# Optimization experiments

Measured on AMD Instinct MI355X. Metric: run time of the kernel, lower is better.

Reference implementation:

```python
import jax, jax.numpy as jnp
import numpy as np

# Config from the repo: 128^3 volume, patch 2 -> 64^3 patches, embed_dim 64
D = H = W = 64
C = 64
WS = 2        # window_size
SS = 1        # shift_size
NH = 8        # num_heads
MLP = 256     # num_mlp
B = 2
L = D * H * W
S = WS ** 3   # tokens per window = 8
NUM_REL = (2 * WS - 1) ** 3  # 27


def _rel_position_index(ws):
    # faithful to source, incl. np.meshgrid default 'xy' indexing
    coords = np.stack(np.meshgrid(np.arange(ws), np.arange(ws), np.arange(ws)))
    cf = coords.reshape(3, -1)
    rc = (cf[:, :, None] - cf[:, None, :]).transpose(1, 2, 0)
    rc[:, :, 0] += ws - 1
    rc[:, :, 1] += ws - 1
    rc[:, :, 2] += ws - 1
    rc[:, :, 0] *= 2 * ws - 1
    return rc.sum(-1)  # (S, S) int


def _attn_mask(d, h, w, ws, ss):
    sl = (slice(0, -ws), slice(-ws, -ss), slice(-ss, None))
    m = np.zeros((1, d, h, w, 1), np.float32)
    cnt = 0
    for ds in sl:
        for hs in sl:
            for wsl in sl:
                m[:, ds, hs, wsl, :] = cnt
                cnt += 1
    pz, py, px = d // ws, h // ws, w // ws
    mw = m.reshape(1, pz, ws, py, ws, px, ws, 1)
    mw = mw.transpose(0, 1, 3, 5, 2, 4, 6, 7).reshape(-1, ws ** 3)  # (nW, S)
    am = mw[:, None, :] - mw[:, :, None]
    return np.where(am != 0, -100.0, 0.0).astype(np.float32)  # (nW, S, S)


_REL_IDX = _rel_position_index(WS).reshape(-1)          # (S*S,)
_MASK = _attn_mask(D, H, W, WS, SS)                     # (nW, S, S)


def setup_inputs() -> dict:
    key = jax.random.key(0)
    ks = jax.random.split(key, 8)
    n = lambda k, s: jax.random.normal(k, s, jnp.float32) * 0.02
    return {
        "x": jax.random.normal(ks[0], (B, L, C), jnp.float32),
        "norm1_g": jnp.ones((C,), jnp.float32),
        "norm1_b": jnp.zeros((C,), jnp.float32),
        "qkv_w": n(ks[1], (C, 3 * C)),
        "qkv_b": jnp.zeros((3 * C,), jnp.float32),
        "rpb": n(ks[2], (NUM_REL, NH)),
        "proj_w": n(ks[3], (C, C)),
        "proj_b": jnp.zeros((C,), jnp.float32),
        "norm2_g": jnp.ones((C,), jnp.float32),
        "norm2_b": jnp.zeros((C,), jnp.float32),
        "mlp_w1": n(ks[4], (C, MLP)),
        "mlp_b1": jnp.zeros((MLP,), jnp.float32),
        "mlp_w2": n(ks[5], (MLP, C)),
        "mlp_b2": jnp.zeros((C,), jnp.float32),
    }


def _ln(x, g, b, eps=1e-5):
    mu = jnp.mean(x, -1, keepdims=True)
    var = jnp.mean(jnp.square(x - mu), -1, keepdims=True)
    return (x - mu) * jax.lax.rsqrt(var + eps) * g + b


def _forward(x, norm1_g, norm1_b, qkv_w, qkv_b, rpb, proj_w, proj_b,
             norm2_g, norm2_b, mlp_w1, mlp_b1, mlp_w2, mlp_b2):
    b = x.shape[0]
    pz, py, px = D // WS, H // WS, W // WS
    hd = C // NH
    scale = hd ** -0.5

    h = _ln(x, norm1_g, norm1_b).reshape(b, D, H, W, C)
    h = jnp.roll(h, (-SS, -SS, -SS), (1, 2, 3))  # cyclic shift
    # window partition -> (b*nW, S, C)
    w = h.reshape(b, pz, WS, py, WS, px, WS, C)
    w = w.transpose(0, 1, 3, 5, 2, 4, 6, 7).reshape(-1, S, C)
    n = w.shape[0]

    qkv = (w @ qkv_w + qkv_b).reshape(n, S, 3, NH, hd).transpose(2, 0, 3, 1, 4)
    q, k, v = qkv[0] * scale, qkv[1], qkv[2]   # (n, NH, S, hd)
    attn = jnp.einsum('nhqd,nhkd->nhqk', q, k)  # (n, NH, S, S)

    # relative position bias, gather + reshape exactly as in the source
    bias = rpb[jnp.asarray(_REL_IDX)].reshape(S, S, S, -1).transpose(3, 0, 1, 2)
    attn = attn + bias  # broadcasts since NH == S == 8 in this config

    mask = jnp.asarray(_MASK)  # (nW, S, S)
    nW = mask.shape[0]
    attn = attn.reshape(-1, nW, NH, S, S) + mask[None, :, None]
    attn = jax.nn.softmax(attn.reshape(-1, NH, S, S), axis=-1)

    out = jnp.einsum('nhqk,nhkd->nhqd', attn, v)
    out = out.transpose(0, 2, 1, 3).reshape(n, S, C)
    out = out @ proj_w + proj_b

    # window reverse (bug-faithful to the source's reshape/transpose order)
    xr = out.reshape(-1, pz, WS, py, px, WS, WS, C)
    xr = xr.transpose(0, 1, 3, 5, 2, 4, 6, 7).reshape(-1, D, H, W, C)
    xr = jnp.roll(xr, (SS, SS, SS), (1, 2, 3))
    h = xr.reshape(b, L, C)

    x = x + h  # DropPath/Dropout are identity in eval mode
    skip = x
    h = _ln(x, norm2_g, norm2_b)
    h = jax.nn.gelu(h @ mlp_w1 + mlp_b1, approximate=False) @ mlp_w2 + mlp_b2
    return skip + h


def reference(x, norm1_g, norm1_b, qkv_w, qkv_b, rpb, proj_w, proj_b,
              norm2_g, norm2_b, mlp_w1, mlp_b1, mlp_w2, mlp_b2):
    return _forward(x, norm1_g, norm1_b, qkv_w, qkv_b, rpb, proj_w, proj_b,
                    norm2_g, norm2_b, mlp_w1, mlp_b1, mlp_w2, mlp_b2)
```

## Files before the change

kernel.cpp:

```cpp
#include <hip/hip_runtime.h>
#include <math.h>

typedef unsigned short u16;
typedef unsigned int u32;
typedef __attribute__((ext_vector_type(8))) short short8;
typedef __attribute__((ext_vector_type(4))) float f32x4;

__device__ __forceinline__ float bf2f(u16 u) {
  union { u32 i; float f; } v; v.i = ((u32)u) << 16; return v.f;
}
__device__ __forceinline__ u16 f2bf(float f) {
  union { float f; u32 i; } v; v.f = f;
  u32 i = v.i;
  i += 0x7fffu + ((i >> 16) & 1u);
  return (u16)(i >> 16);
}

template<bool F32>
__device__ __forceinline__ float ld(const void* p, int i) {
  if (F32) return ((const float*)p)[i];
  return bf2f(((const u16*)p)[i]);
}

__global__ __launch_bounds__(64)
void detect_kernel(const void* __restrict__ xv, int* __restrict__ flag) {
  const u32* xw = (const u32*)xv;
  const int t = threadIdx.x;
  int bad = 0;
  for (int i = t; i < 1024; i += 64) {
    const int e = (int)((xw[i] >> 7) & 0xFF);
    if (e < 90 || e > 150) bad++;
  }
#pragma unroll
  for (int m = 1; m < 64; m <<= 1) bad += __shfl_xor(bad, m);
  if (t == 0) *flag = (bad > 256) ? 1 : 0;
}

template<bool F32>
__device__ __forceinline__ void gather8(const void* __restrict__ x, int chunk,
                                        int w, int s, int cg, float* pf) {
  const int b     = chunk >> 13;
  const int wbase = (chunk & 8191) << 2;
  const int widx  = wbase + w;
  const int wz = widx >> 10, wy = (widx >> 5) & 31, wx = widx & 31;
  const int od = (2*wz + ((s>>2)&1) + 1) & 63;
  const int oh = (2*wy + ((s>>1)&1) + 1) & 63;
  const int ow = (2*wx + ( s    &1) + 1) & 63;
  const int base = (((b<<18) + ((od<<12)|(oh<<6)|ow)) << 6) + cg*8;
  if (F32) {
    const f32x4 a = *(const f32x4*)((const float*)x + base);
    const f32x4 c = *(const f32x4*)((const float*)x + base + 4);
    pf[0]=a[0]; pf[1]=a[1]; pf[2]=a[2]; pf[3]=a[3];
    pf[4]=c[0]; pf[5]=c[1]; pf[6]=c[2]; pf[7]=c[3];
  } else {
    const short8 a = *(const short8*)((const u16*)x + base);
#pragma unroll
    for (int j = 0; j < 8; ++j) pf[j] = bf2f((u16)a[j]);
  }
}

__device__ __forceinline__ int scat(int chunk, int tok) {
  const int b     = chunk >> 13;
  const int wbase = (chunk & 8191) << 2;
  const int widx = wbase + (tok >> 3);
  const int s    = tok & 7;
  const int wz = widx >> 10, wy = (widx >> 5) & 31, wx = widx & 31;
  const int fd = (2*wz + ((wy>>3)&1) + 1) & 63;
  const int Hb = 8*(wy&7) + 4*(wx>>4) + (wy>>4);
  const int Wb = 4*(wx&15);
  const int i = (s>>2)&1, j = (s>>1)&1, k = s&1;
  const int fh = (Hb + 2*j + 1) & 63;
  const int fw = (Wb + 2*i + k + 1) & 63;
  return ((b<<18) + ((fd<<12)|(fh<<6)|fw)) << 6;
}

#define MFMA __builtin_amdgcn_mfma_f32_16x16x32_bf16

template<bool F32>
__device__ __forceinline__ void attn_body(
    const void* __restrict__ x,
    const void* __restrict__ n1g, const void* __restrict__ n1b,
    const void* __restrict__ qkvw, const void* __restrict__ qkvb,
    const void* __restrict__ rpb,
    const void* __restrict__ projw, const void* __restrict__ projb,
    float* __restrict__ out,
    u16* __restrict__ aL, u16* __restrict__ qL,
    u16* __restrict__ kL, u16* __restrict__ vL)
{
  const int tid  = threadIdx.x;
  const int w    = tid >> 6, l = tid & 63;
  const int quad = l >> 4,  col = l & 15;
  const int s8   = l >> 3,  cg  = l & 7;

  float g1v[8], be1v[8];
#pragma unroll
  for (int j = 0; j < 8; ++j) {
    g1v[j]  = ld<F32>(n1g, cg*8 + j);
    be1v[j] = ld<F32>(n1b, cg*8 + j);
  }

  short8 bq[3][2];
#pragma unroll
  for (int nt = 0; nt < 3; ++nt)
#pragma unroll
    for (int kt = 0; kt < 2; ++kt) {
      short8 f;
#pragma unroll
      for (int j = 0; j < 8; ++j)
        f[j] = (short)f2bf(ld<F32>(qkvw, (kt*32 + quad*8 + j)*192 + w*48 + nt*16 + col));
      bq[nt][kt] = f;
    }
  float qb[3];
#pragma unroll
  for (int nt = 0; nt < 3; ++nt) qb[nt] = ld<F32>(qkvb, w*48 + nt*16 + col);
  short8 bp[2];
#pragma unroll
  for (int kt = 0; kt < 2; ++kt) {
    short8 f;
#pragma unroll
    for (int j = 0; j < 8; ++j)
      f[j] = (short)f2bf(ld<F32>(projw, (kt*32 + quad*8 + j)*64 + w*16 + col));
    bp[kt] = f;
  }
  const float pbv = ld<F32>(projb, w*16 + col);
  const int rel = 3 * (((s8>>1)&1) - ((cg>>1)&1) + 1)
                +     (((s8>>2)&1) - ((cg>>2)&1) + 1)
                +     (( s8    &1) - ( cg    &1) + 1);
  float rpv[8];
#pragma unroll
  for (int kk = 0; kk < 8; ++kk) rpv[kk] = ld<F32>(rpb, rel*8 + kk);

  float pf[8];
  gather8<F32>(x, blockIdx.x, w, s8, cg, pf);

  for (int chunk = blockIdx.x; chunk < 16384; chunk += 2048) {
    const int wbase = (chunk & 8191) << 2;
    const int widx0 = wbase + w;
    const int wz0 = widx0 >> 10, wy0 = (widx0 >> 5) & 31, wx0 = widx0 & 31;

    {
      float s1 = 0.f, sq = 0.f;
#pragma unroll
      for (int j = 0; j < 8; ++j) { s1 += pf[j]; sq += pf[j]*pf[j]; }
#pragma unroll
      for (int m = 1; m < 8; m <<= 1) {
        s1 += __shfl_xor(s1, m);
        sq += __shfl_xor(sq, m);
      }
      const float mu  = s1 * 0.015625f;
      const float var = sq * 0.015625f - mu * mu;
      const float rs  = rsqrtf(var + 1e-5f);
      short8 av;
#pragma unroll
      for (int j = 0; j < 8; ++j)
        av[j] = (short)f2bf((pf[j] - mu) * rs * g1v[j] + be1v[j]);
      *(short8*)&aL[(w*8 + s8)*72 + cg*8] = av;
    }
    if (chunk + 2048 < 16384) gather8<F32>(x, chunk + 2048, w, s8, cg, pf);
    __syncthreads();

    {
      short8 aF[2][2];
#pragma unroll
      for (int mt = 0; mt < 2; ++mt)
#pragma unroll
        for (int kt = 0; kt < 2; ++kt)
          aF[mt][kt] = *(const short8*)&aL[(mt*16 + col)*72 + kt*32 + quad*8];
#pragma unroll
      for (int nt = 0; nt < 3; ++nt) {
        f32x4 a0 = (f32x4){0.f,0.f,0.f,0.f}, a1 = (f32x4){0.f,0.f,0.f,0.f};
        a0 = MFMA(aF[0][0], bq[nt][0], a0, 0, 0, 0);
        a0 = MFMA(aF[0][1], bq[nt][1], a0, 0, 0, 0);
        a1 = MFMA(aF[1][0], bq[nt][0], a1, 0, 0, 0);
        a1 = MFMA(aF[1][1], bq[nt][1], a1, 0, 0, 0);
        const int nb  = w*48 + nt*16;
        u16* dst      = (nb < 64) ? qL : (nb < 128) ? kL : vL;
        const int chb = (nb & 63) + col;
        const float scl = (nb < 64) ? 0.35355339059327373f : 1.0f;
        const float bb  = qb[nt];
#pragma unroll
        for (int r = 0; r < 4; ++r) {
          dst[(quad*4 + r)*72 + chb]      = f2bf((a0[r] + bb) * scl);
          dst[(16 + quad*4 + r)*72 + chb] = f2bf((a1[r] + bb) * scl);
        }
      }
    }
    __syncthreads();

    {
      const int tq = w*8 + cg;
      float qr[8];
      {
        const short8 qv = *(const short8*)&qL[tq*72 + s8*8];
#pragma unroll
        for (int d = 0; d < 8; ++d) qr[d] = bf2f((u16)qv[d]);
      }
      float sc8[8];
#pragma unroll
      for (int kk = 0; kk < 8; ++kk) {
        const short8 kv = *(const short8*)&kL[(w*8 + kk)*72 + s8*8];
        float a = 0.f;
#pragma unroll
        for (int d = 0; d < 8; ++d) a += qr[d] * bf2f((u16)kv[d]);
        sc8[kk] = a + rpv[kk];
      }
      {
        int cnts[8];
#pragma unroll
        for (int p = 0; p < 8; ++p) {
          const int sd = 2*wz0 + ((p>>2)&1);
          const int sh = 2*wy0 + ((p>>1)&1);
          const int sw = 2*wx0 + (p&1);
          cnts[p] = (sd >= 62 ? sd - 61 : 0)*9 + (sh >= 62 ? sh - 61 : 0)*3
                  + (sw >= 62 ? sw - 61 : 0);
        }
#pragma unroll
        for (int kk = 0; kk < 8; ++kk)
          if (cnts[kk] != cnts[cg]) sc8[kk] -= 100.f;
      }
      float mx = sc8[0];
#pragma unroll
      for (int kk = 1; kk < 8; ++kk) mx = fmaxf(mx, sc8[kk]);
      float pr[8], lsum = 0.f;
#pragma unroll
      for (int kk = 0; kk < 8; ++kk) { pr[kk] = __expf(sc8[kk] - mx); lsum += pr[kk]; }
      const float inv = __builtin_amdgcn_rcpf(lsum);
      float o[8];
#pragma unroll
      for (int d = 0; d < 8; ++d) o[d] = 0.f;
#pragma unroll
      for (int kk = 0; kk < 8; ++kk) {
        const short8 vv = *(const short8*)&vL[(w*8 + kk)*72 + s8*8];
#pragma unroll
        for (int d = 0; d < 8; ++d) o[d] += pr[kk] * bf2f((u16)vv[d]);
      }
      short8 ov;
#pragma unroll
      for (int d = 0; d < 8; ++d) ov[d] = (short)f2bf(o[d] * inv);
      *(short8*)&qL[tq*72 + s8*8] = ov;
    }
    int offs[8]; float xr[8];
#pragma unroll
    for (int mt = 0; mt < 2; ++mt)
#pragma unroll
      for (int r = 0; r < 4; ++r) {
        const int off = scat(chunk, mt*16 + quad*4 + r) + w*16 + col;
        offs[mt*4 + r] = off;
        xr[mt*4 + r]   = ld<F32>(x, off);
      }
    __syncthreads();

    {
      f32x4 c0 = (f32x4){0.f,0.f,0.f,0.f}, c1 = (f32x4){0.f,0.f,0.f,0.f};
      c0 = MFMA(*(const short8*)&qL[(col)*72 + quad*8],         bp[0], c0, 0, 0, 0);
      c0 = MFMA(*(const short8*)&qL[(col)*72 + 32 + quad*8],    bp[1], c0, 0, 0, 0);
      c1 = MFMA(*(const short8*)&qL[(16+col)*72 + quad*8],      bp[0], c1, 0, 0, 0);
      c1 = MFMA(*(const short8*)&qL[(16+col)*72 + 32 + quad*8], bp[1], c1, 0, 0, 0);
#pragma unroll
      for (int r = 0; r < 4; ++r) {
        out[offs[r]]     = xr[r]     + c0[r] + pbv;
        out[offs[4 + r]] = xr[4 + r] + c1[r] + pbv;
      }
    }
    __syncthreads();
  }
}

__global__ __launch_bounds__(256, 4)
void attn_kernel(const void* __restrict__ x,
                 const void* __restrict__ n1g, const void* __restrict__ n1b,
                 const void* __restrict__ qkvw, const void* __restrict__ qkvb,
                 const void* __restrict__ rpb,
                 const void* __restrict__ projw, const void* __restrict__ projb,
                 const int* __restrict__ flag, float* __restrict__ out)
{
  __shared__ __align__(16) u16 aL[32*72];
  __shared__ __align__(16) u16 qL[32*72];
  __shared__ __align__(16) u16 kL[32*72];
  __shared__ __align__(16) u16 vL[32*72];
  if (*flag)
    attn_body<true >(x, n1g, n1b, qkvw, qkvb, rpb, projw, projb, out, aL, qL, kL, vL);
  else
    attn_body<false>(x, n1g, n1b, qkvw, qkvb, rpb, projw, projb, out, aL, qL, kL, vL);
}

template<bool F32>
__device__ __forceinline__ void mlp_body(
    float* __restrict__ io,
    const void* __restrict__ n2g, const void* __restrict__ n2b,
    const void* __restrict__ mw1, const void* __restrict__ mb1,
    const void* __restrict__ mw2, const void* __restrict__ mb2,
    u16* __restrict__ aL, u16* __restrict__ hL, float* __restrict__ yL)
{
  const int tid  = threadIdx.x;
  const int w    = tid >> 6, l = tid & 63;
  const int quad = l >> 4,  col = l & 15;
  const int s8   = l >> 3,  cg  = l & 7;
  const int ltok = w*8 + s8;
  const int chunk = blockIdx.x;

  float pf[8];
  {
    const float* p = &io[(chunk*32 + ltok)*64 + cg*8];
    const f32x4 a = *(const f32x4*)p;
    const f32x4 c = *(const f32x4*)(p + 4);
    pf[0]=a[0]; pf[1]=a[1]; pf[2]=a[2]; pf[3]=a[3];
    pf[4]=c[0]; pf[5]=c[1]; pf[6]=c[2]; pf[7]=c[3];
  }

  float g2v[8], be2v[8];
#pragma unroll
  for (int j = 0; j < 8; ++j) {
    g2v[j]  = ld<F32>(n2g, cg*8 + j);
    be2v[j] = ld<F32>(n2b, cg*8 + j);
  }
  float b1vv[4];
#pragma unroll
  for (int nt = 0; nt < 4; ++nt) b1vv[nt] = ld<F32>(mb1, w*64 + nt*16 + col);
  const float b2vv = ld<F32>(mb2, w*16 + col);

  short8 b1f[2][4];
#pragma unroll
  for (int kt = 0; kt < 2; ++kt)
#pragma unroll
    for (int nt = 0; nt < 4; ++nt) {
      short8 f;
#pragma unroll
      for (int j = 0; j < 8; ++j)
        f[j] = (short)f2bf(ld<F32>(mw1, (kt*32 + quad*8 + j)*256 + w*64 + nt*16 + col));
      b1f[kt][nt] = f;
    }

  {
    float s1 = 0.f, sq = 0.f;
#pragma unroll
    for (int j = 0; j < 8; ++j) { s1 += pf[j]; sq += pf[j]*pf[j]; }
#pragma unroll
    for (int m = 1; m < 8; m <<= 1) {
      s1 += __shfl_xor(s1, m);
      sq += __shfl_xor(sq, m);
    }
    const float mu  = s1 * 0.015625f;
    const float var = sq * 0.015625f - mu * mu;
    const float rs  = rsqrtf(var + 1e-5f);
    short8 av;
#pragma unroll
    for (int j = 0; j < 8; ++j)
      av[j] = (short)f2bf((pf[j] - mu) * rs * g2v[j] + be2v[j]);
    *(short8*)&aL[ltok*72 + cg*8] = av;
    *(f32x4*)&yL[ltok*68 + cg*8]     = (f32x4){pf[0], pf[1], pf[2], pf[3]};
    *(f32x4*)&yL[ltok*68 + cg*8 + 4] = (f32x4){pf[4], pf[5], pf[6], pf[7]};
  }
  __syncthreads();

  {
    short8 aF[2][2];
#pragma unroll
    for (int mt = 0; mt < 2; ++mt)
#pragma unroll
      for (int kt = 0; kt < 2; ++kt)
        aF[mt][kt] = *(const short8*)&aL[(mt*16 + col)*72 + kt*32 + quad*8];
#pragma unroll
    for (int nt = 0; nt < 4; ++nt) {
      f32x4 m0 = (f32x4){0.f,0.f,0.f,0.f}, m1 = (f32x4){0.f,0.f,0.f,0.f};
      m0 = MFMA(aF[0][0], b1f[0][nt], m0, 0, 0, 0);
      m0 = MFMA(aF[0][1], b1f[1][nt], m0, 0, 0, 0);
      m1 = MFMA(aF[1][0], b1f[0][nt], m1, 0, 0, 0);
      m1 = MFMA(aF[1][1], b1f[1][nt], m1, 0, 0, 0);
      const float bb = b1vv[nt];
#pragma unroll
      for (int r = 0; r < 4; ++r) {
        {
          const float h = m0[r] + bb;
          const float u = h * (1.5957691216f + 0.0713548162f * (h * h));
          const float e = __expf(u);
          hL[(quad*4 + r)*264 + w*64 + nt*16 + col] =
              f2bf(h - h * __builtin_amdgcn_rcpf(e + 1.f));
        }
        {
          const float h = m1[r] + bb;
          const float u = h * (1.5957691216f + 0.0713548162f * (h * h));
          const float e = __expf(u);
          hL[(16 + quad*4 + r)*264 + w*64 + nt*16 + col] =
              f2bf(h - h * __builtin_amdgcn_rcpf(e + 1.f));
        }
      }
    }
  }

  short8 b2f[8];
#pragma unroll
  for (int kt = 0; kt < 8; ++kt) {
    short8 f;
#pragma unroll
    for (int j = 0; j < 8; ++j)
      f[j] = (short)f2bf(ld<F32>(mw2, (kt*32 + quad*8 + j)*64 + w*16 + col));
    b2f[kt] = f;
  }
  __syncthreads();

  {
    f32x4 o0 = (f32x4){0.f,0.f,0.f,0.f}, o1 = (f32x4){0.f,0.f,0.f,0.f};
#pragma unroll
    for (int kt = 0; kt < 8; ++kt) {
      o0 = MFMA(*(const short8*)&hL[(col)*264 + kt*32 + quad*8],    b2f[kt], o0, 0, 0, 0);
      o1 = MFMA(*(const short8*)&hL[(16+col)*264 + kt*32 + quad*8], b2f[kt], o1, 0, 0, 0);
    }
#pragma unroll
    for (int r = 0; r < 4; ++r) {
      const int r0 = quad*4 + r, r1 = 16 + quad*4 + r;
      io[(chunk*32 + r0)*64 + w*16 + col] = yL[r0*68 + w*16 + col] + o0[r] + b2vv;
      io[(chunk*32 + r1)*64 + w*16 + col] = yL[r1*68 + w*16 + col] + o1[r] + b2vv;
    }
  }
}

__global__ __launch_bounds__(256, 4)
void mlp_kernel(float* __restrict__ io,
                const void* __restrict__ n2g, const void* __restrict__ n2b,
                const void* __restrict__ mw1, const void* __restrict__ mb1,
                const void* __restrict__ mw2, const void* __restrict__ mb2,
                const int* __restrict__ flag)
{
  __shared__ __align__(16) u16   aL[32 * 72];
  __shared__ __align__(16) u16   hL[32 * 264];
  __shared__ __align__(16) float yL[32 * 68];
  if (*flag)
    mlp_body<true >(io, n2g, n2b, mw1, mb1, mw2, mb2, aL, hL, yL);
  else
    mlp_body<false>(io, n2g, n2b, mw1, mb1, mw2, mb2, aL, hL, yL);
}

extern "C" void kernel_launch(void* const* d_in, const int* in_sizes, int n_in,
                              void* d_out, int out_size, void* d_ws, size_t ws_size,
                              hipStream_t stream) {
  const void* x     = d_in[0];
  const void* n1g   = d_in[1];
  const void* n1b   = d_in[2];
  const void* qkvw  = d_in[3];
  const void* qkvb  = d_in[4];
  const void* rpb   = d_in[5];
  const void* projw = d_in[6];
  const void* projb = d_in[7];
  const void* n2g   = d_in[8];
  const void* n2b   = d_in[9];
  const void* mw1   = d_in[10];
  const void* mb1   = d_in[11];
  const void* mw2   = d_in[12];
  const void* mb2   = d_in[13];
  float* out = (float*)d_out;
  int* flag  = (int*)d_ws;

  detect_kernel<<<dim3(1), dim3(64), 0, stream>>>(x, flag);
  attn_kernel<<<dim3(2048), dim3(256), 0, stream>>>(
      x, n1g, n1b, qkvw, qkvb, rpb, projw, projb, flag, out);
  mlp_kernel<<<dim3(16384), dim3(256), 0, stream>>>(
      out, n2g, n2b, mw1, mb1, mw2, mb2, flag);
}
```

Before: 459.1 us.

## Prepack MLP weights to bf16 fragments and move residual add into MLP

```diff
diff --git a/kernel.cpp b/kernel.cpp
--- a/kernel.cpp
+++ b/kernel.cpp
@@ -34,6 +34,34 @@
 #pragma unroll
   for (int m = 1; m < 64; m <<= 1) bad += __shfl_xor(bad, m);
   if (t == 0) *flag = (bad > 256) ? 1 : 0;
+}
+
+template<bool F32>
+__device__ __forceinline__ void pack_body(const void* __restrict__ mw1,
+                                          const void* __restrict__ mw2,
+                                          u16* __restrict__ wsb1,
+                                          u16* __restrict__ wsb2) {
+  const int g  = blockIdx.x * 256 + threadIdx.x;
+  const int gs = gridDim.x * 256;
+  for (int e = g; e < 16384; e += gs) {
+    const int j = e & 7, l = (e >> 3) & 63, nt = (e >> 9) & 3,
+              kt = (e >> 11) & 1, w = e >> 12;
+    const int quad = l >> 4, col = l & 15;
+    wsb1[e] = f2bf(ld<F32>(mw1, (kt*32 + quad*8 + j)*256 + w*64 + nt*16 + col));
+  }
+  for (int e = g; e < 16384; e += gs) {
+    const int j = e & 7, l = (e >> 3) & 63, kt = (e >> 9) & 7, w = e >> 12;
+    const int quad = l >> 4, col = l & 15;
+    wsb2[e] = f2bf(ld<F32>(mw2, (kt*32 + quad*8 + j)*64 + w*16 + col));
+  }
+}
+
+__global__ __launch_bounds__(256)
+void pack_kernel(const void* __restrict__ mw1, const void* __restrict__ mw2,
+                 u16* __restrict__ wsb1, u16* __restrict__ wsb2,
+                 const int* __restrict__ flag) {
+  if (*flag) pack_body<true >(mw1, mw2, wsb1, wsb2);
+  else       pack_body<false>(mw1, mw2, wsb1, wsb2);
 }
 
 template<bool F32>
@@ -239,15 +267,12 @@
       for (int d = 0; d < 8; ++d) ov[d] = (short)f2bf(o[d] * inv);
       *(short8*)&qL[tq*72 + s8*8] = ov;
     }
-    int offs[8]; float xr[8];
+    int offs[8];
 #pragma unroll
     for (int mt = 0; mt < 2; ++mt)
 #pragma unroll
-      for (int r = 0; r < 4; ++r) {
-        const int off = scat(chunk, mt*16 + quad*4 + r) + w*16 + col;
-        offs[mt*4 + r] = off;
-        xr[mt*4 + r]   = ld<F32>(x, off);
-      }
+      for (int r = 0; r < 4; ++r)
+        offs[mt*4 + r] = scat(chunk, mt*16 + quad*4 + r) + w*16 + col;
     __syncthreads();
 
     {
@@ -258,11 +283,10 @@
       c1 = MFMA(*(const short8*)&qL[(16+col)*72 + 32 + quad*8], bp[1], c1, 0, 0, 0);
 #pragma unroll
       for (int r = 0; r < 4; ++r) {
-        out[offs[r]]     = xr[r]     + c0[r] + pbv;
-        out[offs[4 + r]] = xr[4 + r] + c1[r] + pbv;
-      }
-    }
-    __syncthreads();
+        out[offs[r]]     = c0[r] + pbv;
+        out[offs[4 + r]] = c1[r] + pbv;
+      }
+    }
   }
 }
 
@@ -284,12 +308,13 @@
     attn_body<false>(x, n1g, n1b, qkvw, qkvb, rpb, projw, projb, out, aL, qL, kL, vL);
 }
 
-template<bool F32>
+template<bool F32, bool PACKED>
 __device__ __forceinline__ void mlp_body(
-    float* __restrict__ io,
+    const void* __restrict__ x, float* __restrict__ io,
     const void* __restrict__ n2g, const void* __restrict__ n2b,
     const void* __restrict__ mw1, const void* __restrict__ mb1,
     const void* __restrict__ mw2, const void* __restrict__ mb2,
+    const u16* __restrict__ wsb1, const u16* __restrict__ wsb2,
     u16* __restrict__ aL, u16* __restrict__ hL, float* __restrict__ yL)
 {
   const int tid  = threadIdx.x;
@@ -299,13 +324,26 @@
   const int ltok = w*8 + s8;
   const int chunk = blockIdx.x;
 
-  float pf[8];
+  float ao[8], xr[8];
   {
     const float* p = &io[(chunk*32 + ltok)*64 + cg*8];
     const f32x4 a = *(const f32x4*)p;
     const f32x4 c = *(const f32x4*)(p + 4);
-    pf[0]=a[0]; pf[1]=a[1]; pf[2]=a[2]; pf[3]=a[3];
-    pf[4]=c[0]; pf[5]=c[1]; pf[6]=c[2]; pf[7]=c[3];
+    ao[0]=a[0]; ao[1]=a[1]; ao[2]=a[2]; ao[3]=a[3];
+    ao[4]=c[0]; ao[5]=c[1]; ao[6]=c[2]; ao[7]=c[3];
+  }
+  {
+    const int base = (chunk*32 + ltok)*64 + cg*8;
+    if (F32) {
+      const f32x4 a = *(const f32x4*)((const float*)x + base);
+      const f32x4 c = *(const f32x4*)((const float*)x + base + 4);
+      xr[0]=a[0]; xr[1]=a[1]; xr[2]=a[2]; xr[3]=a[3];
+      xr[4]=c[0]; xr[5]=c[1]; xr[6]=c[2]; xr[7]=c[3];
+    } else {
+      const short8 a = *(const short8*)((const u16*)x + base);
+#pragma unroll
+      for (int j = 0; j < 8; ++j) xr[j] = bf2f((u16)a[j]);
+    }
   }
 
   float g2v[8], be2v[8];
@@ -324,17 +362,24 @@
   for (int kt = 0; kt < 2; ++kt)
 #pragma unroll
     for (int nt = 0; nt < 4; ++nt) {
-      short8 f;
-#pragma unroll
-      for (int j = 0; j < 8; ++j)
-        f[j] = (short)f2bf(ld<F32>(mw1, (kt*32 + quad*8 + j)*256 + w*64 + nt*16 + col));
-      b1f[kt][nt] = f;
+      if (PACKED) {
+        b1f[kt][nt] = *(const short8*)&wsb1[((((w*2 + kt)*4 + nt)*64) + l)*8];
+      } else {
+        short8 f;
+#pragma unroll
+        for (int j = 0; j < 8; ++j)
+          f[j] = (short)f2bf(ld<F32>(mw1, (kt*32 + quad*8 + j)*256 + w*64 + nt*16 + col));
+        b1f[kt][nt] = f;
+      }
     }
 
   {
+    float yv[8];
+#pragma unroll
+    for (int j = 0; j < 8; ++j) yv[j] = xr[j] + ao[j];
     float s1 = 0.f, sq = 0.f;
 #pragma unroll
-    for (int j = 0; j < 8; ++j) { s1 += pf[j]; sq += pf[j]*pf[j]; }
+    for (int j = 0; j < 8; ++j) { s1 += yv[j]; sq += yv[j]*yv[j]; }
 #pragma unroll
     for (int m = 1; m < 8; m <<= 1) {
       s1 += __shfl_xor(s1, m);
@@ -346,10 +391,10 @@
     short8 av;
 #pragma unroll
     for (int j = 0; j < 8; ++j)
-      av[j] = (short)f2bf((pf[j] - mu) * rs * g2v[j] + be2v[j]);
+      av[j] = (short)f2bf((yv[j] - mu) * rs * g2v[j] + be2v[j]);
     *(short8*)&aL[ltok*72 + cg*8] = av;
-    *(f32x4*)&yL[ltok*68 + cg*8]     = (f32x4){pf[0], pf[1], pf[2], pf[3]};
-    *(f32x4*)&yL[ltok*68 + cg*8 + 4] = (f32x4){pf[4], pf[5], pf[6], pf[7]};
+    *(f32x4*)&yL[ltok*68 + cg*8]     = (f32x4){yv[0], yv[1], yv[2], yv[3]};
+    *(f32x4*)&yL[ltok*68 + cg*8 + 4] = (f32x4){yv[4], yv[5], yv[6], yv[7]};
   }
   __syncthreads();
 
@@ -391,11 +436,15 @@
   short8 b2f[8];
 #pragma unroll
   for (int kt = 0; kt < 8; ++kt) {
-    short8 f;
-#pragma unroll
-    for (int j = 0; j < 8; ++j)
-      f[j] = (short)f2bf(ld<F32>(mw2, (kt*32 + quad*8 + j)*64 + w*16 + col));
-    b2f[kt] = f;
+    if (PACKED) {
+      b2f[kt] = *(const short8*)&wsb2[(((w*8 + kt)*64) + l)*8];
+    } else {
+      short8 f;
+#pragma unroll
+      for (int j = 0; j < 8; ++j)
+        f[j] = (short)f2bf(ld<F32>(mw2, (kt*32 + quad*8 + j)*64 + w*16 + col));
+      b2f[kt] = f;
+    }
   }
   __syncthreads();
 
@@ -415,20 +464,22 @@
   }
 }
 
+template<bool PACKED>
 __global__ __launch_bounds__(256, 4)
-void mlp_kernel(float* __restrict__ io,
+void mlp_kernel(const void* __restrict__ x, float* __restrict__ io,
                 const void* __restrict__ n2g, const void* __restrict__ n2b,
                 const void* __restrict__ mw1, const void* __restrict__ mb1,
                 const void* __restrict__ mw2, const void* __restrict__ mb2,
+                const u16* __restrict__ wsb1, const u16* __restrict__ wsb2,
                 const int* __restrict__ flag)
 {
   __shared__ __align__(16) u16   aL[32 * 72];
   __shared__ __align__(16) u16   hL[32 * 264];
   __shared__ __align__(16) float yL[32 * 68];
   if (*flag)
-    mlp_body<true >(io, n2g, n2b, mw1, mb1, mw2, mb2, aL, hL, yL);
+    mlp_body<true , PACKED>(x, io, n2g, n2b, mw1, mb1, mw2, mb2, wsb1, wsb2, aL, hL, yL);
   else
-    mlp_body<false>(io, n2g, n2b, mw1, mb1, mw2, mb2, aL, hL, yL);
+    mlp_body<false, PACKED>(x, io, n2g, n2b, mw1, mb1, mw2, mb2, wsb1, wsb2, aL, hL, yL);
 }
 
 extern "C" void kernel_launch(void* const* d_in, const int* in_sizes, int n_in,
@@ -450,10 +501,19 @@
   const void* mb2   = d_in[13];
   float* out = (float*)d_out;
   int* flag  = (int*)d_ws;
+  u16* wsb1  = (u16*)((char*)d_ws + 64);
+  u16* wsb2  = wsb1 + 16384;
+  const bool packed = ws_size >= (size_t)(64 + 2*16384*2);
 
   detect_kernel<<<dim3(1), dim3(64), 0, stream>>>(x, flag);
+  if (packed)
+    pack_kernel<<<dim3(16), dim3(256), 0, stream>>>(mw1, mw2, wsb1, wsb2, flag);
   attn_kernel<<<dim3(2048), dim3(256), 0, stream>>>(
       x, n1g, n1b, qkvw, qkvb, rpb, projw, projb, flag, out);
-  mlp_kernel<<<dim3(16384), dim3(256), 0, stream>>>(
-      out, n2g, n2b, mw1, mb1, mw2, mb2, flag);
-}
+  if (packed)
+    mlp_kernel<true ><<<dim3(16384), dim3(256), 0, stream>>>(
+        x, out, n2g, n2b, mw1, mb1, mw2, mb2, wsb1, wsb2, flag);
+  else
+    mlp_kernel<false><<<dim3(16384), dim3(256), 0, stream>>>(
+        x, out, n2g, n2b, mw1, mb1, mw2, mb2, wsb1, wsb2, flag);
+}
```

Result: faster. 414.5 us (-9.7%).
